# Kernel optimization log

Hardware: AMD Instinct MI355X
Metric: run time of the kernel (lower is better)

The kernel has to match this reference:

```python
import jax, jax.numpy as jnp
import numpy as np

B, NQ, D, NH, L, P = 8, 1000, 256, 8, 4, 4
DFF = 1024
HD = D // NH
SHAPES = np.array([[128, 128], [64, 64], [32, 32], [16, 16]], dtype=np.int64)
S = int((SHAPES[:, 0] * SHAPES[:, 1]).sum())  # 21760
LEVEL_START = np.concatenate([np.zeros(1, np.int64), np.cumsum(SHAPES[:, 0] * SHAPES[:, 1])[:-1]])


def setup_inputs() -> dict:
    key = jax.random.key(0)
    ks = jax.random.split(key, 20)
    w = lambda k, shape, s=0.02: jax.random.normal(k, shape, jnp.float32) * s
    z = lambda n: jnp.zeros((n,), jnp.float32)
    return dict(
        query=w(ks[0], (B, NQ, D), 1.0),
        query_pos=w(ks[1], (B, NQ, D), 1.0),
        reference_points=jax.random.uniform(ks[2], (B, NQ, L, 4), jnp.float32),
        input_flatten=w(ks[3], (B, S, D), 1.0),
        input_spatial_shapes=SHAPES,
        input_level_start_index=LEVEL_START,
        Wq=w(ks[4], (D, D)), bq=z(D), Wk=w(ks[5], (D, D)), bk=z(D),
        Wv=w(ks[6], (D, D)), bv=z(D), Wo=w(ks[7], (D, D)), bo=z(D),
        ln1_g=jnp.ones((D,), jnp.float32), ln1_b=z(D),
        W_off=w(ks[8], (D, NH * L * P * 2)), b_off=z(NH * L * P * 2),
        W_attn=w(ks[9], (D, NH * L * P)), b_attn=z(NH * L * P),
        W_val=w(ks[10], (D, D)), b_val=z(D),
        W_cout=w(ks[11], (D, D)), b_cout=z(D),
        ln2_g=jnp.ones((D,), jnp.float32), ln2_b=z(D),
        W1=w(ks[12], (D, DFF)), b1=z(DFF),
        W2=w(ks[13], (DFF, D)), b2=z(D),
        ln3_g=jnp.ones((D,), jnp.float32), ln3_b=z(D),
    )


def layer_norm(x, g, b, eps=1e-5):
    mu = x.mean(-1, keepdims=True)
    var = ((x - mu) ** 2).mean(-1, keepdims=True)
    return (x - mu) / jnp.sqrt(var + eps) * g + b


def _ms_deform(value, shapes_np, loc, aw):
    # value: (B,S,NH,HD); loc: (B,Nq,NH,L,P,2) in [0,1]; aw: (B,Nq,NH,L,P)
    Bz, _, nh, hd = value.shape
    Nq = loc.shape[1]
    awt = aw.transpose(0, 2, 1, 3, 4)  # (B,NH,Nq,L,P)
    acc = jnp.zeros((Bz, nh, Nq, hd), value.dtype)
    start = 0
    for lvl in range(shapes_np.shape[0]):
        Hl, Wl = int(shapes_np[lvl, 0]), int(shapes_np[lvl, 1])
        vf = value[:, start:start + Hl * Wl].transpose(0, 2, 1, 3)  # (B,NH,Hl*Wl,HD)
        start += Hl * Wl
        # grid_sample align_corners=False: pixel coord = loc * size - 0.5
        lx = loc[:, :, :, lvl, :, 0].transpose(0, 2, 1, 3) * Wl - 0.5  # (B,NH,Nq,P)
        ly = loc[:, :, :, lvl, :, 1].transpose(0, 2, 1, 3) * Hl - 0.5
        x0 = jnp.floor(lx); y0 = jnp.floor(ly)
        tx = lx - x0; ty = ly - y0
        x0i = x0.astype(jnp.int32); y0i = y0.astype(jnp.int32)

        def gather(xi, yi):
            valid = (xi >= 0) & (xi < Wl) & (yi >= 0) & (yi < Hl)
            idx = jnp.clip(yi, 0, Hl - 1) * Wl + jnp.clip(xi, 0, Wl - 1)
            out = jnp.take_along_axis(vf, idx.reshape(Bz, nh, Nq * P)[..., None], axis=2)
            return out.reshape(Bz, nh, Nq, P, hd) * valid[..., None]

        g00 = gather(x0i, y0i)
        g01 = gather(x0i + 1, y0i)
        g10 = gather(x0i, y0i + 1)
        g11 = gather(x0i + 1, y0i + 1)
        samp = (g00 * ((1 - tx) * (1 - ty))[..., None] + g01 * (tx * (1 - ty))[..., None]
                + g10 * ((1 - tx) * ty)[..., None] + g11 * (tx * ty)[..., None])  # (B,NH,Nq,P,HD)
        acc = acc + jnp.einsum('bhqp,bhqpd->bhqd', awt[:, :, :, lvl], samp)
    return acc.transpose(0, 2, 1, 3).reshape(Bz, Nq, nh * hd)


def reference(query, query_pos, reference_points, input_flatten, input_spatial_shapes,
              input_level_start_index, Wq, bq, Wk, bk, Wv, bv, Wo, bo, ln1_g, ln1_b,
              W_off, b_off, W_attn, b_attn, W_val, b_val, W_cout, b_cout, ln2_g, ln2_b,
              W1, b1, W2, b2, ln3_g, ln3_b):
    Bz, Nq, Dm = query.shape
    # --- self-attention (post-norm), pos added to Q/K only ---
    qp = query + query_pos
    q = (qp @ Wq + bq).reshape(Bz, Nq, NH, HD)
    k = (qp @ Wk + bk).reshape(Bz, Nq, NH, HD)
    v = (query @ Wv + bv).reshape(Bz, Nq, NH, HD)
    att = jax.nn.softmax(jnp.einsum('bqhd,bkhd->bhqk', q, k) / jnp.sqrt(jnp.float32(HD)), axis=-1)
    sa = jnp.einsum('bhqk,bkhd->bqhd', att, v).reshape(Bz, Nq, Dm) @ Wo + bo
    x = layer_norm(query + sa, ln1_g, ln1_b)
    # --- deformable cross-attention ---
    q2 = x + query_pos
    value = (input_flatten @ W_val + b_val).reshape(Bz, -1, NH, HD)
    off = (q2 @ W_off + b_off).reshape(Bz, Nq, NH, L, P, 2)
    aw = jax.nn.softmax((q2 @ W_attn + b_attn).reshape(Bz, Nq, NH, L * P), axis=-1)
    aw = aw.reshape(Bz, Nq, NH, L, P)
    rp = reference_points  # (B,Nq,L,4) cxcywh
    loc = rp[:, :, None, :, None, :2] + off / P * rp[:, :, None, :, None, 2:] * 0.5
    shapes_np = np.asarray(input_spatial_shapes)
    ca = _ms_deform(value, shapes_np, loc, aw) @ W_cout + b_cout
    x = layer_norm(x + ca, ln2_g, ln2_b)
    # --- FFN ---
    ffn = jax.nn.relu(x @ W1 + b1) @ W2 + b2
    return layer_norm(x + ffn, ln3_g, ln3_b)
```

## Files before the change

kernel.cpp:

```cpp
#include <hip/hip_runtime.h>
#include <hip/hip_bf16.h>

#define B_   8
#define NQ_  1000
#define D_   256
#define NH_  8
#define L_   4
#define P_   4
#define DFF_ 1024
#define HD_  32
#define S_   21760
#define NTOK (B_*NQ_)

typedef short  bf16x8 __attribute__((ext_vector_type(8)));
typedef float  f32x4  __attribute__((ext_vector_type(4)));

#define WAITBAR(N) asm volatile("s_waitcnt vmcnt(" #N ") lgkmcnt(0)\n\ts_barrier" ::: "memory")
#define ENDBAR()   asm volatile("s_barrier" ::: "memory")

__device__ inline unsigned short f32_to_bf16_bits(float f) {
    unsigned int u = __float_as_uint(f);
    unsigned int rounding = 0x7FFFu + ((u >> 16) & 1u);
    u += rounding;
    return (unsigned short)(u >> 16);
}
__device__ inline float bf16_bits_to_f32(unsigned short b) {
    return __uint_as_float(((unsigned int)b) << 16);
}
__device__ inline unsigned int pack_trunc(float f0, float f1) {
    return __builtin_amdgcn_perm(__float_as_uint(f1), __float_as_uint(f0), 0x07060302u);
}
__device__ inline void async_copy16(const void* g, void* l) {
    __builtin_amdgcn_global_load_lds((const __attribute__((address_space(1))) unsigned int*)g,
                                     (__attribute__((address_space(3))) unsigned int*)l, 16, 0, 0);
}

__global__ __launch_bounds__(256) void vgemm(const float* __restrict__ Af,
                                             const unsigned short* __restrict__ Bt,
                                             const float* __restrict__ bias,
                                             unsigned short* __restrict__ Cb)
{
    constexpr int K = 256;
    constexpr int N = 256;
    __shared__ __align__(16) unsigned short sA[128 * 64];
    __shared__ __align__(16) unsigned short sB[2][128 * 64];
    const int tid = threadIdx.x;
    const int w = tid >> 6, l = tid & 63;
    const int n0 = blockIdx.x * 128, m0 = blockIdx.y * 128;
    const int wr = w >> 1, wc = w & 1;

    f32x4 acc[4][4];
    #pragma unroll
    for (int i = 0; i < 4; i++)
        #pragma unroll
        for (int j = 0; j < 4; j++)
            #pragma unroll
            for (int r = 0; r < 4; r++) acc[i][j][r] = 0.f;

    const int lrow = (tid >> 3);
    const int lko  = (tid & 7) * 8;

    auto issueB = [&](int t, int buf) {
        #pragma unroll
        for (int r = 0; r < 4; r++) {
            int boff = ((r * 4 + w) * 64 + l) * 16;
            int row  = boff >> 7;
            int kb   = (boff & 127) ^ ((row & 7) << 4);
            async_copy16(Bt + (size_t)(n0 + row) * K + t * 64 + (kb >> 1),
                         sB[buf] + (size_t)(r * 4 + w) * 512);
        }
    };
    auto loadA = [&](int t, float4* fr) {
        #pragma unroll
        for (int r = 0; r < 4; r++) {
            int row = r * 32 + lrow;
            const float* ap = Af + (size_t)(m0 + row) * K + t * 64 + lko;
            fr[r * 2]     = *reinterpret_cast<const float4*>(ap);
            fr[r * 2 + 1] = *reinterpret_cast<const float4*>(ap + 4);
        }
    };
    auto writeA = [&](const float4* fr) {
        #pragma unroll
        for (int r = 0; r < 4; r++) {
            int row = r * 32 + lrow;
            float4 a0 = fr[r * 2], a1 = fr[r * 2 + 1];
            uint4 t4;
            t4.x = pack_trunc(a0.x, a0.y);
            t4.y = pack_trunc(a0.z, a0.w);
            t4.z = pack_trunc(a1.x, a1.y);
            t4.w = pack_trunc(a1.z, a1.w);
            int sw = (lko * 2) ^ ((row & 7) << 4);
            *reinterpret_cast<uint4*>(&sA[row * 64 + (sw >> 1)]) = t4;
        }
    };
    auto compute = [&](int buf) {
        const unsigned short* sBc = sB[buf];
        #pragma unroll
        for (int kk = 0; kk < 2; kk++) {
            bf16x8 afr[4], bfr[4];
            const int kbyte = kk * 64 + ((l >> 4) << 4);
            #pragma unroll
            for (int mi = 0; mi < 4; mi++) {
                int row = wr * 64 + mi * 16 + (l & 15);
                int sw = kbyte ^ ((row & 7) << 4);
                afr[mi] = *reinterpret_cast<const bf16x8*>(&sA[row * 64 + (sw >> 1)]);
            }
            #pragma unroll
            for (int ni = 0; ni < 4; ni++) {
                int row = wc * 64 + ni * 16 + (l & 15);
                int sw = kbyte ^ ((row & 7) << 4);
                bfr[ni] = *reinterpret_cast<const bf16x8*>(&sBc[row * 64 + (sw >> 1)]);
            }
            #pragma unroll
            for (int mi = 0; mi < 4; mi++)
                #pragma unroll
                for (int ni = 0; ni < 4; ni++)
                    acc[mi][ni] = __builtin_amdgcn_mfma_f32_16x16x32_bf16(
                        afr[mi], bfr[ni], acc[mi][ni], 0, 0, 0);
        }
    };

    float4 frA[8], frB[8];

    loadA(0, frA);
    issueB(0, 0);
    loadA(1, frB);

    writeA(frA);
    issueB(1, 1);
    loadA(2, frA);
    WAITBAR(20);
    compute(0);
    ENDBAR();
    writeA(frB);
    issueB(2, 0);
    loadA(3, frB);
    WAITBAR(20);
    compute(1);
    ENDBAR();
    writeA(frA);
    issueB(3, 1);
    WAITBAR(12);
    compute(0);
    ENDBAR();
    writeA(frB);
    WAITBAR(0);
    compute(1);
    ENDBAR();

    #pragma unroll
    for (int mi = 0; mi < 4; mi++) {
        #pragma unroll
        for (int ni = 0; ni < 4; ni++) {
            int col = n0 + wc * 64 + ni * 16 + (l & 15);
            float bz = bias[col];
            #pragma unroll
            for (int rg = 0; rg < 4; rg++) {
                int row = m0 + wr * 64 + mi * 16 + ((l >> 4) << 2) + rg;
                Cb[(size_t)row * N + col] = f32_to_bf16_bits(acc[mi][ni][rg] + bz);
            }
        }
    }
}

template<int AMODE, bool RELU, int CMODE, int BN, int K, int NSTRIP>
__global__ __launch_bounds__(256) void bgemm(const void* __restrict__ Av,
                                             const float* __restrict__ A2,
                                             const unsigned short* __restrict__ Bt,
                                             const float* __restrict__ bias,
                                             float* __restrict__ Cf,
                                             unsigned short* __restrict__ Cb,
                                             int N)
{
    constexpr int NF   = BN / 16;
    constexpr int KF   = K / 32;
    constexpr int ROWB = K * 2;
    constexpr int FILL = BN * ROWB / 4096;

    __shared__ __align__(16) unsigned short sB[BN * K];

    const int tid = threadIdx.x;
    const int w = tid >> 6, l = tid & 63;
    const int g = l >> 4, lr = l & 15;
    const int n0 = blockIdx.x * BN;

    const unsigned short* Ab = (const unsigned short*)Av;
    const float* Af = (const float*)Av;

    #pragma unroll
    for (int r = 0; r < FILL; r++) {
        int lin = (r * 256 + tid) * 16;
        int row = lin / ROWB;
        int kb  = (lin & (ROWB - 1)) ^ ((row & 7) << 4);
        async_copy16(Bt + (size_t)(n0 + row) * K + (kb >> 1), (char*)sB + lin);
    }
    asm volatile("s_waitcnt vmcnt(0)\n\ts_barrier" ::: "memory");

    float bz[NF];
    #pragma unroll
    for (int nf = 0; nf < NF; nf++) bz[nf] = bias[n0 + nf * 16 + lr];

    for (int s = 0; s < NSTRIP; s++) {
        const int m0w = (blockIdx.y * NSTRIP + s) * 64 + w * 16;
        const int arow = m0w + lr;

        f32x4 acc[NF];
        #pragma unroll
        for (int nf = 0; nf < NF; nf++)
            #pragma unroll
            for (int r = 0; r < 4; r++) acc[nf][r] = 0.f;

        #pragma unroll
        for (int kf = 0; kf < KF; kf++) {
            bf16x8 af;
            if constexpr (AMODE == 0) {
                af = *reinterpret_cast<const bf16x8*>(Ab + (size_t)arow * K + kf * 32 + g * 8);
            } else {
                const float* ap = Af + (size_t)arow * K + kf * 32 + g * 8;
                float4 a0 = *reinterpret_cast<const float4*>(ap);
                float4 a1 = *reinterpret_cast<const float4*>(ap + 4);
                if constexpr (AMODE == 2) {
                    const float* a2 = A2 + (size_t)arow * K + kf * 32 + g * 8;
                    float4 b0 = *reinterpret_cast<const float4*>(a2);
                    float4 b1 = *reinterpret_cast<const float4*>(a2 + 4);
                    a0.x += b0.x; a0.y += b0.y; a0.z += b0.z; a0.w += b0.w;
                    a1.x += b1.x; a1.y += b1.y; a1.z += b1.z; a1.w += b1.w;
                }
                uint4 t;
                t.x = pack_trunc(a0.x, a0.y);
                t.y = pack_trunc(a0.z, a0.w);
                t.z = pack_trunc(a1.x, a1.y);
                t.w = pack_trunc(a1.z, a1.w);
                af = *reinterpret_cast<bf16x8*>(&t);
            }
            #pragma unroll
            for (int nf = 0; nf < NF; nf++) {
                int brow = nf * 16 + lr;
                bf16x8 bf = *reinterpret_cast<const bf16x8*>(
                    (const char*)sB + brow * ROWB + ((kf * 64 + g * 16) ^ ((brow & 7) << 4)));
                acc[nf] = __builtin_amdgcn_mfma_f32_16x16x32_bf16(af, bf, acc[nf], 0, 0, 0);
            }
        }

        #pragma unroll
        for (int nf = 0; nf < NF; nf++) {
            int col = n0 + nf * 16 + lr;
            if constexpr (CMODE == 2) {
                int row0 = m0w + g * 4;
                int bb = row0 / 1000;
                int key = row0 - bb * 1000;
                ushort4 q4;
                q4.x = f32_to_bf16_bits(acc[nf][0] + bz[nf]);
                q4.y = f32_to_bf16_bits(acc[nf][1] + bz[nf]);
                q4.z = f32_to_bf16_bits(acc[nf][2] + bz[nf]);
                q4.w = f32_to_bf16_bits(acc[nf][3] + bz[nf]);
                *reinterpret_cast<ushort4*>(Cb + (size_t)bb * 262144 + (size_t)col * 1024 + key) = q4;
            } else {
                #pragma unroll
                for (int rg = 0; rg < 4; rg++) {
                    int row = m0w + g * 4 + rg;
                    float v = acc[nf][rg] + bz[nf];
                    if (RELU) v = fmaxf(v, 0.f);
                    if constexpr (CMODE == 1)
                        Cb[(size_t)row * N + col] = f32_to_bf16_bits(v);
                    else
                        Cf[(size_t)row * N + col] = v;
                }
            }
        }
    }
}

struct WJobs {
    const float* src[10];
    unsigned short* dst[10];
    int K[10], N[10];
};
__global__ __launch_bounds__(256) void wconv_k(WJobs j)
{
    const int job = blockIdx.y;
    const int K = j.K[job], N = j.N[job];
    const int tilesN = N >> 6;
    const int ntiles = (K >> 6) * tilesN;
    const int tile = blockIdx.x;
    if (tile >= ntiles) return;
    const int kt = tile / tilesN, nt = tile - kt * tilesN;
    const int k0 = kt * 64, n0 = nt * 64;
    __shared__ unsigned short t_[64][65];
    const float* src = j.src[job];
    unsigned short* dst = j.dst[job];
    const int cc = threadIdx.x & 63, rr = threadIdx.x >> 6;
    #pragma unroll
    for (int i = 0; i < 16; i++) {
        int k = i * 4 + rr;
        t_[k][cc] = f32_to_bf16_bits(src[(size_t)(k0 + k) * N + n0 + cc]);
    }
    __syncthreads();
    #pragma unroll
    for (int i = 0; i < 16; i++) {
        int n = i * 4 + rr;
        dst[(size_t)(n0 + n) * K + k0 + cc] = t_[cc][n];
    }
}

__global__ __launch_bounds__(1024) void biaspack_k(const float* bq, const float* bk,
                                                   const float* boff, const float* battn,
                                                   float* qkb, float* oab)
{
    int t = threadIdx.x;
    if (t < 256)      qkb[t] = bq[t];
    else if (t < 512) qkb[t] = bk[t - 256];
    else if (t < 768) oab[t - 512] = boff[t - 512];
    else if (t < 896) oab[t - 512] = battn[t - 768];
}

__global__ __launch_bounds__(256) void fattn_k(const unsigned short* __restrict__ qk,
                                               const unsigned short* __restrict__ vt,
                                               unsigned short* __restrict__ sa)
{
    const int b = blockIdx.z, h = blockIdx.y;
    const int tid = threadIdx.x;
    const int w = tid >> 6, l = tid & 63;
    const int lq = l & 15, g = l >> 4;
    const int q0 = blockIdx.x * 64 + w * 16;

    __shared__ __align__(16) unsigned short Ks[2][128 * 32];
    __shared__ __align__(16) unsigned short Vs[2][32 * 128];
    __shared__ __align__(16) unsigned short Ps[4][16 * 128];

    int qrow = q0 + lq; if (qrow > NQ_ - 1) qrow = NQ_ - 1;
    const bf16x8 qfrag = *reinterpret_cast<const bf16x8*>(
        qk + ((size_t)(b * NQ_ + qrow)) * 512 + h * 32 + g * 8);

    f32x4 O0 = {0.f, 0.f, 0.f, 0.f}, O1 = {0.f, 0.f, 0.f, 0.f};
    float m = -1e30f, lsum = 0.f;
    const float scale = 0.17677669529663687f;

    const size_t kbase = (size_t)b * (NQ_ * 512) + 256 + h * 32;
    const size_t vbase = (size_t)b * 262144 + (size_t)(h * 32) * 1024;
    const int swz = (lq & 7) << 4;

    auto issueKV = [&](int kt, int buf) {
        #pragma unroll
        for (int r = 0; r < 2; r++) {
            int lin = (r * 256 + tid) * 16;
            int krow = lin >> 6;
            int kb = (lin & 63) ^ ((krow & 7) << 4);
            async_copy16(qk + kbase + (size_t)(kt * 128 + krow) * 512 + (kb >> 1),
                         (char*)Ks[buf] + lin);
            int d = lin >> 8;
            int vb = (lin & 255) ^ ((d & 7) << 4);
            async_copy16(vt + vbase + (size_t)d * 1024 + kt * 128 + (vb >> 1),
                         (char*)Vs[buf] + lin);
        }
    };

    issueKV(0, 0);

    for (int kt = 0; kt < 8; kt++) {
        const int k0 = kt * 128;
        const int cur = kt & 1;
        asm volatile("s_waitcnt vmcnt(0) lgkmcnt(0)\n\ts_barrier" ::: "memory");
        if (kt < 7) issueKV(kt + 1, cur ^ 1);

        const unsigned short* Kc = Ks[cur];
        const unsigned short* Vc = Vs[cur];

        float t[8][4];
        float tmax = -1e30f;
        const bool tail = (k0 + 128 > NQ_);
        #pragma unroll
        for (int ni = 0; ni < 8; ni++) {
            int row = ni * 16 + lq;
            bf16x8 kf = *reinterpret_cast<const bf16x8*>(
                (const char*)Kc + row * 64 + ((g * 16) ^ swz));
            f32x4 st = __builtin_amdgcn_mfma_f32_16x16x32_bf16(
                kf, qfrag, (f32x4){0.f, 0.f, 0.f, 0.f}, 0, 0, 0);
            #pragma unroll
            for (int rg = 0; rg < 4; rg++) {
                float tv = st[rg] * scale;
                if (tail) {
                    int key = k0 + ni * 16 + g * 4 + rg;
                    tv = (key < NQ_) ? tv : -1e30f;
                }
                t[ni][rg] = tv;
                tmax = fmaxf(tmax, tv);
            }
        }
        tmax = fmaxf(tmax, __shfl_xor(tmax, 16));
        tmax = fmaxf(tmax, __shfl_xor(tmax, 32));
        float mnew = fmaxf(m, tmax);
        float corr = __expf(m - mnew);
        m = mnew;

        float rs = 0.f;
        unsigned int pk[8][2];
        #pragma unroll
        for (int ni = 0; ni < 8; ni++) {
            float p0 = __expf(t[ni][0] - mnew);
            float p1 = __expf(t[ni][1] - mnew);
            float p2 = __expf(t[ni][2] - mnew);
            float p3 = __expf(t[ni][3] - mnew);
            rs += (p0 + p1) + (p2 + p3);
            pk[ni][0] = ((unsigned)f32_to_bf16_bits(p0)) | (((unsigned)f32_to_bf16_bits(p1)) << 16);
            pk[ni][1] = ((unsigned)f32_to_bf16_bits(p2)) | (((unsigned)f32_to_bf16_bits(p3)) << 16);
        }
        rs += __shfl_xor(rs, 16);
        rs += __shfl_xor(rs, 32);
        lsum = lsum * corr + rs;

        float c0 = __shfl(corr, g * 4 + 0);
        float c1 = __shfl(corr, g * 4 + 1);
        float c2 = __shfl(corr, g * 4 + 2);
        float c3 = __shfl(corr, g * 4 + 3);
        O0[0] *= c0; O0[1] *= c1; O0[2] *= c2; O0[3] *= c3;
        O1[0] *= c0; O1[1] *= c1; O1[2] *= c2; O1[3] *= c3;

        unsigned short* Pw = Ps[w];
        #pragma unroll
        for (int ni = 0; ni < 8; ni++) {
            int byteoff = lq * 256 + ((ni * 32 + g * 8) ^ swz);
            *reinterpret_cast<uint2*>((char*)Pw + byteoff) = make_uint2(pk[ni][0], pk[ni][1]);
        }

        #pragma unroll
        for (int c = 0; c < 4; c++) {
            int rb = (c * 64 + g * 16) ^ swz;
            bf16x8 pa = *reinterpret_cast<const bf16x8*>((const char*)Pw + lq * 256 + rb);
            bf16x8 v0 = *reinterpret_cast<const bf16x8*>((const char*)Vc + lq * 256 + rb);
            bf16x8 v1 = *reinterpret_cast<const bf16x8*>((const char*)Vc + (16 + lq) * 256 + rb);
            O0 = __builtin_amdgcn_mfma_f32_16x16x32_bf16(pa, v0, O0, 0, 0, 0);
            O1 = __builtin_amdgcn_mfma_f32_16x16x32_bf16(pa, v1, O1, 0, 0, 0);
        }
    }

    float linv = 1.f / lsum;
    float i0 = __shfl(linv, g * 4 + 0);
    float i1 = __shfl(linv, g * 4 + 1);
    float i2 = __shfl(linv, g * 4 + 2);
    float i3 = __shfl(linv, g * 4 + 3);
    float iv[4] = {i0, i1, i2, i3};
    #pragma unroll
    for (int rg = 0; rg < 4; rg++) {
        int qg = q0 + g * 4 + rg;
        if (qg < NQ_) {
            size_t obase = ((size_t)(b * NQ_ + qg)) * 256 + h * 32;
            sa[obase + lq]      = f32_to_bf16_bits(O0[rg] * iv[rg]);
            sa[obase + 16 + lq] = f32_to_bf16_bits(O1[rg] * iv[rg]);
        }
    }
}

__global__ __launch_bounds__(256) void ln_k(const float* __restrict__ a,
                                            const float* __restrict__ bsum,
                                            const float* __restrict__ g,
                                            const float* __restrict__ be,
                                            float* __restrict__ out)
{
    const int wave = threadIdx.x >> 6, lane = threadIdx.x & 63;
    const int row = blockIdx.x * 4 + wave;
    float4 xa = reinterpret_cast<const float4*>(a + (size_t)row * 256)[lane];
    float4 xb = reinterpret_cast<const float4*>(bsum + (size_t)row * 256)[lane];
    float4 x = {xa.x + xb.x, xa.y + xb.y, xa.z + xb.z, xa.w + xb.w};
    float s  = x.x + x.y + x.z + x.w;
    float ss = x.x * x.x + x.y * x.y + x.z * x.z + x.w * x.w;
    #pragma unroll
    for (int off = 32; off > 0; off >>= 1) {
        s  += __shfl_xor(s, off);
        ss += __shfl_xor(ss, off);
    }
    float mu  = s * (1.f / 256.f);
    float var = ss * (1.f / 256.f) - mu * mu;
    float rstd = rsqrtf(var + 1e-5f);
    float4 gv = reinterpret_cast<const float4*>(g)[lane];
    float4 bv = reinterpret_cast<const float4*>(be)[lane];
    float4 o = {(x.x - mu) * rstd * gv.x + bv.x,
                (x.y - mu) * rstd * gv.y + bv.y,
                (x.z - mu) * rstd * gv.z + bv.z,
                (x.w - mu) * rstd * gv.w + bv.w};
    reinterpret_cast<float4*>(out + (size_t)row * 256)[lane] = o;
}

__device__ inline unsigned int samp2(const unsigned short* __restrict__ v,
                                     int b, int st, int Wl, int Hl,
                                     int x, int y, int hc)
{
    bool valid = (x >= 0) & (x < Wl) & (y >= 0) & (y < Hl);
    int xc = min(max(x, 0), Wl - 1);
    int yc = min(max(y, 0), Hl - 1);
    size_t idx = ((size_t)(b * S_ + st + yc * Wl + xc)) * 256 + hc;
    unsigned int val = *reinterpret_cast<const unsigned int*>(v + idx);
    return valid ? val : 0u;
}

__global__ __launch_bounds__(256) void deform_k(const float* __restrict__ rp,
                                                const float* __restrict__ oa,
                                                const unsigned short* __restrict__ value,
                                                unsigned short* __restrict__ ca)
{
    const int tk = threadIdx.x >> 7;
    const int tok = blockIdx.x * 2 + tk;
    const int b = tok / NQ_;
    const int h = (threadIdx.x >> 4) & 7;
    const int cp = threadIdx.x & 15;
    const int hc = h * 32 + cp * 2;

    const float* awp = oa + (size_t)tok * 384 + 256 + h * 16;
    float w[16];
    float mx = -1e30f;
    #pragma unroll
    for (int i = 0; i < 16; i++) { w[i] = awp[i]; mx = fmaxf(mx, w[i]); }
    float sum = 0.f;
    #pragma unroll
    for (int i = 0; i < 16; i++) { w[i] = __expf(w[i] - mx); sum += w[i]; }
    const float inv = 1.f / sum;

    const float* rpp  = rp + (size_t)tok * (L_ * 4);
    const float* offp = oa + (size_t)tok * 384 + h * 32;

    const int lvlW[4] = {128, 64, 32, 16};
    const int lvlS[4] = {0, 16384, 20480, 21504};

    float acc0 = 0.f, acc1 = 0.f;
    #pragma unroll
    for (int l = 0; l < 4; l++) {
        const int Wl = lvlW[l], Hl = lvlW[l], st = lvlS[l];
        const float cx = rpp[l * 4 + 0], cy = rpp[l * 4 + 1];
        const float cw = rpp[l * 4 + 2], chh = rpp[l * 4 + 3];
        #pragma unroll
        for (int p = 0; p < 4; p++) {
            float ox = offp[l * 8 + p * 2 + 0];
            float oy = offp[l * 8 + p * 2 + 1];
            float lx = (cx + ox * 0.25f * cw * 0.5f) * Wl - 0.5f;
            float ly = (cy + oy * 0.25f * chh * 0.5f) * Hl - 0.5f;
            float x0f = floorf(lx), y0f = floorf(ly);
            float tx = lx - x0f, ty = ly - y0f;
            int x0 = (int)x0f, y0 = (int)y0f;
            unsigned int u00 = samp2(value, b, st, Wl, Hl, x0,     y0,     hc);
            unsigned int u01 = samp2(value, b, st, Wl, Hl, x0 + 1, y0,     hc);
            unsigned int u10 = samp2(value, b, st, Wl, Hl, x0,     y0 + 1, hc);
            unsigned int u11 = samp2(value, b, st, Wl, Hl, x0 + 1, y0 + 1, hc);
            float w00 = (1.f - tx) * (1.f - ty), w01 = tx * (1.f - ty);
            float w10 = (1.f - tx) * ty,         w11 = tx * ty;
            float g0 = bf16_bits_to_f32((unsigned short)u00) * w00
                     + bf16_bits_to_f32((unsigned short)u01) * w01
                     + bf16_bits_to_f32((unsigned short)u10) * w10
                     + bf16_bits_to_f32((unsigned short)u11) * w11;
            float g1 = bf16_bits_to_f32((unsigned short)(u00 >> 16)) * w00
                     + bf16_bits_to_f32((unsigned short)(u01 >> 16)) * w01
                     + bf16_bits_to_f32((unsigned short)(u10 >> 16)) * w10
                     + bf16_bits_to_f32((unsigned short)(u11 >> 16)) * w11;
            float wa = w[l * 4 + p] * inv;
            acc0 += wa * g0;
            acc1 += wa * g1;
        }
    }
    unsigned int packed = ((unsigned)f32_to_bf16_bits(acc0)) | (((unsigned)f32_to_bf16_bits(acc1)) << 16);
    *reinterpret_cast<unsigned int*>(ca + (size_t)tok * 256 + hc) = packed;
}

extern "C" void kernel_launch(void* const* d_in, const int* in_sizes, int n_in,
                              void* d_out, int out_size, void* d_ws, size_t ws_size,
                              hipStream_t stream)
{
    const float* query      = (const float*)d_in[0];
    const float* query_pos  = (const float*)d_in[1];
    const float* ref_pts    = (const float*)d_in[2];
    const float* input_flat = (const float*)d_in[3];
    const float* Wq = (const float*)d_in[6];  const float* bq = (const float*)d_in[7];
    const float* Wk = (const float*)d_in[8];  const float* bk = (const float*)d_in[9];
    const float* Wv = (const float*)d_in[10]; const float* bv = (const float*)d_in[11];
    const float* Wo = (const float*)d_in[12]; const float* bo = (const float*)d_in[13];
    const float* ln1g = (const float*)d_in[14]; const float* ln1b = (const float*)d_in[15];
    const float* W_off = (const float*)d_in[16]; const float* b_off = (const float*)d_in[17];
    const float* W_attn = (const float*)d_in[18]; const float* b_attn = (const float*)d_in[19];
    const float* W_val = (const float*)d_in[20]; const float* b_val = (const float*)d_in[21];
    const float* W_cout = (const float*)d_in[22]; const float* b_cout = (const float*)d_in[23];
    const float* ln2g = (const float*)d_in[24]; const float* ln2b = (const float*)d_in[25];
    const float* W1 = (const float*)d_in[26]; const float* b1 = (const float*)d_in[27];
    const float* W2 = (const float*)d_in[28]; const float* b2 = (const float*)d_in[29];
    const float* ln3g = (const float*)d_in[30]; const float* ln3b = (const float*)d_in[31];
    float* out = (float*)d_out;

    char* base = (char*)d_ws;
    size_t off = 0;
    auto alloc = [&](size_t bytes) { void* p = base + off; off += (bytes + 255) & ~(size_t)255; return p; };
    unsigned short* value_bf = (unsigned short*)alloc((size_t)B_ * S_ * 256 * 2);
    unsigned short* qk_bf = (unsigned short*)alloc((size_t)NTOK * 1024 * 2);
    unsigned short* h_bf = qk_bf;
    unsigned short* vt = (unsigned short*)alloc((size_t)B_ * 256 * 1024 * 2);
    float* oa_buf = (float*)alloc((size_t)NTOK * 384 * 4);
    float* tmp0   = (float*)alloc((size_t)NTOK * 256 * 4);
    float* x1     = (float*)alloc((size_t)NTOK * 256 * 4);
    float* x2     = (float*)alloc((size_t)NTOK * 256 * 4);
    unsigned short* sc_bf = (unsigned short*)alloc((size_t)NTOK * 256 * 2);
    unsigned short* wqk   = (unsigned short*)alloc(512 * 256 * 2);
    unsigned short* wv    = (unsigned short*)alloc(256 * 256 * 2);
    unsigned short* wo    = (unsigned short*)alloc(256 * 256 * 2);
    unsigned short* woa   = (unsigned short*)alloc(384 * 256 * 2);
    unsigned short* wval  = (unsigned short*)alloc(256 * 256 * 2);
    unsigned short* wcout = (unsigned short*)alloc(256 * 256 * 2);
    unsigned short* w1t   = (unsigned short*)alloc(1024 * 256 * 2);
    unsigned short* w2t   = (unsigned short*)alloc(256 * 1024 * 2);
    float* qkbias = (float*)alloc(512 * 4);
    float* oabias = (float*)alloc(384 * 4);

    dim3 blk(256);

    WJobs wj;
    wj.src[0] = Wq;    wj.dst[0] = wqk;               wj.K[0] = 256;  wj.N[0] = 256;
    wj.src[1] = Wk;    wj.dst[1] = wqk + 256 * 256;   wj.K[1] = 256;  wj.N[1] = 256;
    wj.src[2] = Wv;    wj.dst[2] = wv;                wj.K[2] = 256;  wj.N[2] = 256;
    wj.src[3] = Wo;    wj.dst[3] = wo;                wj.K[3] = 256;  wj.N[3] = 256;
    wj.src[4] = W_off; wj.dst[4] = woa;               wj.K[4] = 256;  wj.N[4] = 256;
    wj.src[5] = W_attn;wj.dst[5] = woa + 256 * 256;   wj.K[5] = 256;  wj.N[5] = 128;
    wj.src[6] = W_val; wj.dst[6] = wval;              wj.K[6] = 256;  wj.N[6] = 256;
    wj.src[7] = W_cout;wj.dst[7] = wcout;             wj.K[7] = 256;  wj.N[7] = 256;
    wj.src[8] = W1;    wj.dst[8] = w1t;               wj.K[8] = 256;  wj.N[8] = 1024;
    wj.src[9] = W2;    wj.dst[9] = w2t;               wj.K[9] = 1024; wj.N[9] = 256;
    wconv_k<<<dim3(64, 10), blk, 0, stream>>>(wj);
    biaspack_k<<<1, 1024, 0, stream>>>(bq, bk, b_off, b_attn, qkbias, oabias);

    bgemm<2, false, 1,  64, 256, 1><<<dim3(8, 125), blk, 0, stream>>>(query, query_pos, wqk, qkbias, nullptr, qk_bf, 512);
    bgemm<1, false, 2,  64, 256, 1><<<dim3(4, 125), blk, 0, stream>>>(query, nullptr,   wv,  bv,     nullptr, vt,    256);
    fattn_k<<<dim3(16, NH_, B_), blk, 0, stream>>>(qk_bf, vt, sc_bf);
    bgemm<0, false, 0,  64, 256, 1><<<dim3(4, 125), blk, 0, stream>>>(sc_bf, nullptr, wo, bo, tmp0, nullptr, 256);
    ln_k<<<NTOK / 4, blk, 0, stream>>>(query, tmp0, ln1g, ln1b, x1);

    vgemm<<<dim3(2, 1360), blk, 0, stream>>>(input_flat, wval, b_val, value_bf);
    bgemm<2, false, 0,  64, 256, 1><<<dim3(6, 125), blk, 0, stream>>>(x1, query_pos, woa, oabias, oa_buf, nullptr, 384);
    deform_k<<<NTOK / 2, blk, 0, stream>>>(ref_pts, oa_buf, value_bf, sc_bf);
    bgemm<0, false, 0,  64, 256, 1><<<dim3(4, 125), blk, 0, stream>>>(sc_bf, nullptr, wcout, b_cout, tmp0, nullptr, 256);
    ln_k<<<NTOK / 4, blk, 0, stream>>>(x1, tmp0, ln2g, ln2b, x2);

    bgemm<1, true,  1,  64, 256, 1><<<dim3(16, 125), blk, 0, stream>>>(x2, nullptr, w1t, b1, nullptr, h_bf, 1024);
    bgemm<0, false, 0,  32, 1024, 1><<<dim3(8, 125), blk, 0, stream>>>(h_bf, nullptr, w2t, b2, tmp0, nullptr, 256);
    ln_k<<<NTOK / 4, blk, 0, stream>>>(x2, tmp0, ln3g, ln3b, out);
}
```

Baseline: 278.5 us.

## Pre-convert GEMM activations to bf16 in a merged prep kernel and layernorm epilogues

Adds a single prep kernel that merges weight transposition, bias packing, conversion of input_flatten to bf16, and bf16 conversion of query and query+pos. Layernorm kernels now also emit bf16 copies (x1+pos, x2) for the next GEMM. This lets every GEMM read bf16 A operands directly, and vgemm loads A asynchronously into LDS with a simple double-buffered loop. The aim is to cut fp32 A traffic and in-kernel conversion, at the cost of an extra full pass that writes and rereads a bf16 copy of input_flatten (~89MB).

```diff
diff --git a/kernel.cpp b/kernel.cpp
--- a/kernel.cpp
+++ b/kernel.cpp
@@ -35,14 +35,89 @@
                                      (__attribute__((address_space(3))) unsigned int*)l, 16, 0, 0);
 }
 
-__global__ __launch_bounds__(256) void vgemm(const float* __restrict__ Af,
-                                             const unsigned short* __restrict__ Bt,
-                                             const float* __restrict__ bias,
-                                             unsigned short* __restrict__ Cb)
+struct PrepArgs {
+    const float* wsrc[10];
+    unsigned short* wdst[10];
+    int wK[10], wN[10];
+    const float* bq; const float* bk; const float* boff; const float* battn;
+    float* qkb; float* oab;
+    const float* input_flat; unsigned short* if_bf;
+    const float* query; const float* qpos;
+    unsigned short* q_bf; unsigned short* qp_bf;
+};
+__global__ __launch_bounds__(256) void prep_k(PrepArgs P)
+{
+    const int bid = blockIdx.x, tid = threadIdx.x;
+    if (bid < 640) {
+        const int job = bid >> 6, tile = bid & 63;
+        const int K = P.wK[job], N = P.wN[job];
+        const int tilesN = N >> 6;
+        if (tile >= (K >> 6) * tilesN) return;
+        const int kt = tile / tilesN, nt = tile - kt * tilesN;
+        const int k0 = kt * 64, n0 = nt * 64;
+        __shared__ unsigned short t_[64][65];
+        const float* src = P.wsrc[job];
+        unsigned short* dst = P.wdst[job];
+        const int cc = tid & 63, rr = tid >> 6;
+        #pragma unroll
+        for (int i = 0; i < 16; i++) {
+            int k = i * 4 + rr;
+            t_[k][cc] = f32_to_bf16_bits(src[(size_t)(k0 + k) * N + n0 + cc]);
+        }
+        __syncthreads();
+        #pragma unroll
+        for (int i = 0; i < 16; i++) {
+            int n = i * 4 + rr;
+            dst[(size_t)(n0 + n) * K + k0 + cc] = t_[cc][n];
+        }
+    } else if (bid < 2816) {
+        int idx = (bid - 640) * 256 + tid;
+        for (int i = idx; i < 5570560; i += 2176 * 256) {
+            const float* p = P.input_flat + (size_t)i * 8;
+            float4 a0 = *reinterpret_cast<const float4*>(p);
+            float4 a1 = *reinterpret_cast<const float4*>(p + 4);
+            uint4 t;
+            t.x = pack_trunc(a0.x, a0.y);
+            t.y = pack_trunc(a0.z, a0.w);
+            t.z = pack_trunc(a1.x, a1.y);
+            t.w = pack_trunc(a1.z, a1.w);
+            *reinterpret_cast<uint4*>(P.if_bf + (size_t)i * 8) = t;
+        }
+    } else if (bid == 2816) {
+        P.qkb[tid]       = P.bq[tid];
+        P.qkb[256 + tid] = P.bk[tid];
+        P.oab[tid]       = P.boff[tid];
+        if (tid < 128) P.oab[256 + tid] = P.battn[tid];
+    } else {
+        int idx = (bid - 2817) * 256 + tid;
+        for (int i = idx; i < 256000; i += 64 * 256) {
+            const float* q = P.query + (size_t)i * 8;
+            const float* p = P.qpos  + (size_t)i * 8;
+            float4 q0 = *reinterpret_cast<const float4*>(q);
+            float4 q1 = *reinterpret_cast<const float4*>(q + 4);
+            float4 p0 = *reinterpret_cast<const float4*>(p);
+            float4 p1 = *reinterpret_cast<const float4*>(p + 4);
+            uint4 tq, tp;
+            tq.x = pack_trunc(q0.x, q0.y);       tq.y = pack_trunc(q0.z, q0.w);
+            tq.z = pack_trunc(q1.x, q1.y);       tq.w = pack_trunc(q1.z, q1.w);
+            tp.x = pack_trunc(q0.x + p0.x, q0.y + p0.y);
+            tp.y = pack_trunc(q0.z + p0.z, q0.w + p0.w);
+            tp.z = pack_trunc(q1.x + p1.x, q1.y + p1.y);
+            tp.w = pack_trunc(q1.z + p1.z, q1.w + p1.w);
+            *reinterpret_cast<uint4*>(P.q_bf  + (size_t)i * 8) = tq;
+            *reinterpret_cast<uint4*>(P.qp_bf + (size_t)i * 8) = tp;
+        }
+    }
+}
+
+__global__ __launch_bounds__(256) void vgemm0(const unsigned short* __restrict__ Ab,
+                                              const unsigned short* __restrict__ Bt,
+                                              const float* __restrict__ bias,
+                                              unsigned short* __restrict__ Cb)
 {
     constexpr int K = 256;
     constexpr int N = 256;
-    __shared__ __align__(16) unsigned short sA[128 * 64];
+    __shared__ __align__(16) unsigned short sA[2][128 * 64];
     __shared__ __align__(16) unsigned short sB[2][128 * 64];
     const int tid = threadIdx.x;
     const int w = tid >> 6, l = tid & 63;
@@ -57,9 +132,16 @@
             #pragma unroll
             for (int r = 0; r < 4; r++) acc[i][j][r] = 0.f;
 
-    const int lrow = (tid >> 3);
-    const int lko  = (tid & 7) * 8;
-
+    auto issueA = [&](int t, int buf) {
+        #pragma unroll
+        for (int r = 0; r < 4; r++) {
+            int boff = ((r * 4 + w) * 64 + l) * 16;
+            int row  = boff >> 7;
+            int kb   = (boff & 127) ^ ((row & 7) << 4);
+            async_copy16(Ab + (size_t)(m0 + row) * K + t * 64 + (kb >> 1),
+                         sA[buf] + (size_t)(r * 4 + w) * 512);
+        }
+    };
     auto issueB = [&](int t, int buf) {
         #pragma unroll
         for (int r = 0; r < 4; r++) {
@@ -70,31 +152,19 @@
                          sB[buf] + (size_t)(r * 4 + w) * 512);
         }
     };
-    auto loadA = [&](int t, float4* fr) {
-        #pragma unroll
-        for (int r = 0; r < 4; r++) {
-            int row = r * 32 + lrow;
-            const float* ap = Af + (size_t)(m0 + row) * K + t * 64 + lko;
-            fr[r * 2]     = *reinterpret_cast<const float4*>(ap);
-            fr[r * 2 + 1] = *reinterpret_cast<const float4*>(ap + 4);
-        }
-    };
-    auto writeA = [&](const float4* fr) {
-        #pragma unroll
-        for (int r = 0; r < 4; r++) {
-            int row = r * 32 + lrow;
-            float4 a0 = fr[r * 2], a1 = fr[r * 2 + 1];
-            uint4 t4;
-            t4.x = pack_trunc(a0.x, a0.y);
-            t4.y = pack_trunc(a0.z, a0.w);
-            t4.z = pack_trunc(a1.x, a1.y);
-            t4.w = pack_trunc(a1.z, a1.w);
-            int sw = (lko * 2) ^ ((row & 7) << 4);
-            *reinterpret_cast<uint4*>(&sA[row * 64 + (sw >> 1)]) = t4;
-        }
-    };
-    auto compute = [&](int buf) {
-        const unsigned short* sBc = sB[buf];
+
+    issueA(0, 0);
+    issueB(0, 0);
+
+    for (int t = 0; t < 4; t++) {
+        const int cur = t & 1;
+        if (t + 1 < 4) {
+            issueA(t + 1, cur ^ 1);
+            issueB(t + 1, cur ^ 1);
+            WAITBAR(8);
+        } else {
+            WAITBAR(0);
+        }
         #pragma unroll
         for (int kk = 0; kk < 2; kk++) {
             bf16x8 afr[4], bfr[4];
@@ -103,13 +173,13 @@
             for (int mi = 0; mi < 4; mi++) {
                 int row = wr * 64 + mi * 16 + (l & 15);
                 int sw = kbyte ^ ((row & 7) << 4);
-                afr[mi] = *reinterpret_cast<const bf16x8*>(&sA[row * 64 + (sw >> 1)]);
+                afr[mi] = *reinterpret_cast<const bf16x8*>(&sA[cur][row * 64 + (sw >> 1)]);
             }
             #pragma unroll
             for (int ni = 0; ni < 4; ni++) {
                 int row = wc * 64 + ni * 16 + (l & 15);
                 int sw = kbyte ^ ((row & 7) << 4);
-                bfr[ni] = *reinterpret_cast<const bf16x8*>(&sBc[row * 64 + (sw >> 1)]);
+                bfr[ni] = *reinterpret_cast<const bf16x8*>(&sB[cur][row * 64 + (sw >> 1)]);
             }
             #pragma unroll
             for (int mi = 0; mi < 4; mi++)
@@ -118,35 +188,8 @@
                     acc[mi][ni] = __builtin_amdgcn_mfma_f32_16x16x32_bf16(
                         afr[mi], bfr[ni], acc[mi][ni], 0, 0, 0);
         }
-    };
-
-    float4 frA[8], frB[8];
-
-    loadA(0, frA);
-    issueB(0, 0);
-    loadA(1, frB);
-
-    writeA(frA);
-    issueB(1, 1);
-    loadA(2, frA);
-    WAITBAR(20);
-    compute(0);
-    ENDBAR();
-    writeA(frB);
-    issueB(2, 0);
-    loadA(3, frB);
-    WAITBAR(20);
-    compute(1);
-    ENDBAR();
-    writeA(frA);
-    issueB(3, 1);
-    WAITBAR(12);
-    compute(0);
-    ENDBAR();
-    writeA(frB);
-    WAITBAR(0);
-    compute(1);
-    ENDBAR();
+        ENDBAR();
+    }
 
     #pragma unroll
     for (int mi = 0; mi < 4; mi++) {
@@ -163,9 +206,8 @@
     }
 }
 
-template<int AMODE, bool RELU, int CMODE, int BN, int K, int NSTRIP>
-__global__ __launch_bounds__(256) void bgemm(const void* __restrict__ Av,
-                                             const float* __restrict__ A2,
+template<bool RELU, int CMODE, int BN, int K>
+__global__ __launch_bounds__(256) void bgemm(const unsigned short* __restrict__ Ab,
                                              const unsigned short* __restrict__ Bt,
                                              const float* __restrict__ bias,
                                              float* __restrict__ Cf,
@@ -184,9 +226,6 @@
     const int g = l >> 4, lr = l & 15;
     const int n0 = blockIdx.x * BN;
 
-    const unsigned short* Ab = (const unsigned short*)Av;
-    const float* Af = (const float*)Av;
-
     #pragma unroll
     for (int r = 0; r < FILL; r++) {
         int lin = (r * 256 + tid) * 16;
@@ -200,118 +239,53 @@
     #pragma unroll
     for (int nf = 0; nf < NF; nf++) bz[nf] = bias[n0 + nf * 16 + lr];
 
-    for (int s = 0; s < NSTRIP; s++) {
-        const int m0w = (blockIdx.y * NSTRIP + s) * 64 + w * 16;
-        const int arow = m0w + lr;
-
-        f32x4 acc[NF];
-        #pragma unroll
-        for (int nf = 0; nf < NF; nf++)
+    const int m0w = blockIdx.y * 64 + w * 16;
+    const int arow = m0w + lr;
+
+    f32x4 acc[NF];
+    #pragma unroll
+    for (int nf = 0; nf < NF; nf++)
+        #pragma unroll
+        for (int r = 0; r < 4; r++) acc[nf][r] = 0.f;
+
+    #pragma unroll
+    for (int kf = 0; kf < KF; kf++) {
+        bf16x8 af = *reinterpret_cast<const bf16x8*>(Ab + (size_t)arow * K + kf * 32 + g * 8);
+        #pragma unroll
+        for (int nf = 0; nf < NF; nf++) {
+            int brow = nf * 16 + lr;
+            bf16x8 bf = *reinterpret_cast<const bf16x8*>(
+                (const char*)sB + brow * ROWB + ((kf * 64 + g * 16) ^ ((brow & 7) << 4)));
+            acc[nf] = __builtin_amdgcn_mfma_f32_16x16x32_bf16(af, bf, acc[nf], 0, 0, 0);
+        }
+    }
+
+    #pragma unroll
+    for (int nf = 0; nf < NF; nf++) {
+        int col = n0 + nf * 16 + lr;
+        if constexpr (CMODE == 2) {
+            int row0 = m0w + g * 4;
+            int bb = row0 / 1000;
+            int key = row0 - bb * 1000;
+            ushort4 q4;
+            q4.x = f32_to_bf16_bits(acc[nf][0] + bz[nf]);
+            q4.y = f32_to_bf16_bits(acc[nf][1] + bz[nf]);
+            q4.z = f32_to_bf16_bits(acc[nf][2] + bz[nf]);
+            q4.w = f32_to_bf16_bits(acc[nf][3] + bz[nf]);
+            *reinterpret_cast<ushort4*>(Cb + (size_t)bb * 262144 + (size_t)col * 1024 + key) = q4;
+        } else {
             #pragma unroll
-            for (int r = 0; r < 4; r++) acc[nf][r] = 0.f;
-
-        #pragma unroll
-        for (int kf = 0; kf < KF; kf++) {
-            bf16x8 af;
-            if constexpr (AMODE == 0) {
-                af = *reinterpret_cast<const bf16x8*>(Ab + (size_t)arow * K + kf * 32 + g * 8);
-            } else {
-                const float* ap = Af + (size_t)arow * K + kf * 32 + g * 8;
-                float4 a0 = *reinterpret_cast<const float4*>(ap);
-                float4 a1 = *reinterpret_cast<const float4*>(ap + 4);
-                if constexpr (AMODE == 2) {
-                    const float* a2 = A2 + (size_t)arow * K + kf * 32 + g * 8;
-                    float4 b0 = *reinterpret_cast<const float4*>(a2);
-                    float4 b1 = *reinterpret_cast<const float4*>(a2 + 4);
-                    a0.x += b0.x; a0.y += b0.y; a0.z += b0.z; a0.w += b0.w;
-                    a1.x += b1.x; a1.y += b1.y; a1.z += b1.z; a1.w += b1.w;
-                }
-                uint4 t;
-                t.x = pack_trunc(a0.x, a0.y);
-                t.y = pack_trunc(a0.z, a0.w);
-                t.z = pack_trunc(a1.x, a1.y);
-                t.w = pack_trunc(a1.z, a1.w);
-                af = *reinterpret_cast<bf16x8*>(&t);
+            for (int rg = 0; rg < 4; rg++) {
+                int row = m0w + g * 4 + rg;
+                float v = acc[nf][rg] + bz[nf];
+                if (RELU) v = fmaxf(v, 0.f);
+                if constexpr (CMODE == 1)
+                    Cb[(size_t)row * N + col] = f32_to_bf16_bits(v);
+                else
+                    Cf[(size_t)row * N + col] = v;
             }
-            #pragma unroll
-            for (int nf = 0; nf < NF; nf++) {
-                int brow = nf * 16 + lr;
-                bf16x8 bf = *reinterpret_cast<const bf16x8*>(
-                    (const char*)sB + brow * ROWB + ((kf * 64 + g * 16) ^ ((brow & 7) << 4)));
-                acc[nf] = __builtin_amdgcn_mfma_f32_16x16x32_bf16(af, bf, acc[nf], 0, 0, 0);
-            }
-        }
-
-        #pragma unroll
-        for (int nf = 0; nf < NF; nf++) {
-            int col = n0 + nf * 16 + lr;
-            if constexpr (CMODE == 2) {
-                int row0 = m0w + g * 4;
-                int bb = row0 / 1000;
-                int key = row0 - bb * 1000;
-                ushort4 q4;
-                q4.x = f32_to_bf16_bits(acc[nf][0] + bz[nf]);
-                q4.y = f32_to_bf16_bits(acc[nf][1] + bz[nf]);
-                q4.z = f32_to_bf16_bits(acc[nf][2] + bz[nf]);
-                q4.w = f32_to_bf16_bits(acc[nf][3] + bz[nf]);
-                *reinterpret_cast<ushort4*>(Cb + (size_t)bb * 262144 + (size_t)col * 1024 + key) = q4;
-            } else {
-                #pragma unroll
-                for (int rg = 0; rg < 4; rg++) {
-                    int row = m0w + g * 4 + rg;
-                    float v = acc[nf][rg] + bz[nf];
-                    if (RELU) v = fmaxf(v, 0.f);
-                    if constexpr (CMODE == 1)
-                        Cb[(size_t)row * N + col] = f32_to_bf16_bits(v);
-                    else
-                        Cf[(size_t)row * N + col] = v;
-                }
-            }
-        }
-    }
-}
-
-struct WJobs {
-    const float* src[10];
-    unsigned short* dst[10];
-    int K[10], N[10];
-};
-__global__ __launch_bounds__(256) void wconv_k(WJobs j)
-{
-    const int job = blockIdx.y;
-    const int K = j.K[job], N = j.N[job];
-    const int tilesN = N >> 6;
-    const int ntiles = (K >> 6) * tilesN;
-    const int tile = blockIdx.x;
-    if (tile >= ntiles) return;
-    const int kt = tile / tilesN, nt = tile - kt * tilesN;
-    const int k0 = kt * 64, n0 = nt * 64;
-    __shared__ unsigned short t_[64][65];
-    const float* src = j.src[job];
-    unsigned short* dst = j.dst[job];
-    const int cc = threadIdx.x & 63, rr = threadIdx.x >> 6;
-    #pragma unroll
-    for (int i = 0; i < 16; i++) {
-        int k = i * 4 + rr;
-        t_[k][cc] = f32_to_bf16_bits(src[(size_t)(k0 + k) * N + n0 + cc]);
-    }
-    __syncthreads();
-    #pragma unroll
-    for (int i = 0; i < 16; i++) {
-        int n = i * 4 + rr;
-        dst[(size_t)(n0 + n) * K + k0 + cc] = t_[cc][n];
-    }
-}
-
-__global__ __launch_bounds__(1024) void biaspack_k(const float* bq, const float* bk,
-                                                   const float* boff, const float* battn,
-                                                   float* qkb, float* oab)
-{
-    int t = threadIdx.x;
-    if (t < 256)      qkb[t] = bq[t];
-    else if (t < 512) qkb[t] = bk[t - 256];
-    else if (t < 768) oab[t - 512] = boff[t - 512];
-    else if (t < 896) oab[t - 512] = battn[t - 768];
+        }
+    }
 }
 
 __global__ __launch_bounds__(256) void fattn_k(const unsigned short* __restrict__ qk,
@@ -451,11 +425,14 @@
     }
 }
 
+template<int OM>
 __global__ __launch_bounds__(256) void ln_k(const float* __restrict__ a,
                                             const float* __restrict__ bsum,
+                                            const float* __restrict__ pos,
                                             const float* __restrict__ g,
                                             const float* __restrict__ be,
-                                            float* __restrict__ out)
+                                            float* __restrict__ out,
+                                            unsigned short* __restrict__ outb)
 {
     const int wave = threadIdx.x >> 6, lane = threadIdx.x & 63;
     const int row = blockIdx.x * 4 + wave;
@@ -479,6 +456,18 @@
                 (x.z - mu) * rstd * gv.z + bv.z,
                 (x.w - mu) * rstd * gv.w + bv.w};
     reinterpret_cast<float4*>(out + (size_t)row * 256)[lane] = o;
+    if constexpr (OM == 1) {
+        ushort4 q4;
+        q4.x = f32_to_bf16_bits(o.x); q4.y = f32_to_bf16_bits(o.y);
+        q4.z = f32_to_bf16_bits(o.z); q4.w = f32_to_bf16_bits(o.w);
+        *reinterpret_cast<ushort4*>(outb + (size_t)row * 256 + lane * 4) = q4;
+    } else if constexpr (OM == 2) {
+        float4 pv = reinterpret_cast<const float4*>(pos + (size_t)row * 256)[lane];
+        ushort4 q4;
+        q4.x = f32_to_bf16_bits(o.x + pv.x); q4.y = f32_to_bf16_bits(o.y + pv.y);
+        q4.z = f32_to_bf16_bits(o.z + pv.z); q4.w = f32_to_bf16_bits(o.w + pv.w);
+        *reinterpret_cast<ushort4*>(outb + (size_t)row * 256 + lane * 4) = q4;
+    }
 }
 
 __device__ inline unsigned int samp2(const unsigned short* __restrict__ v,
@@ -586,6 +575,7 @@
     size_t off = 0;
     auto alloc = [&](size_t bytes) { void* p = base + off; off += (bytes + 255) & ~(size_t)255; return p; };
     unsigned short* value_bf = (unsigned short*)alloc((size_t)B_ * S_ * 256 * 2);
+    unsigned short* if_bf = (unsigned short*)alloc((size_t)B_ * S_ * 256 * 2);
     unsigned short* qk_bf = (unsigned short*)alloc((size_t)NTOK * 1024 * 2);
     unsigned short* h_bf = qk_bf;
     unsigned short* vt = (unsigned short*)alloc((size_t)B_ * 256 * 1024 * 2);
@@ -593,7 +583,11 @@
     float* tmp0   = (float*)alloc((size_t)NTOK * 256 * 4);
     float* x1     = (float*)alloc((size_t)NTOK * 256 * 4);
     float* x2     = (float*)alloc((size_t)NTOK * 256 * 4);
-    unsigned short* sc_bf = (unsigned short*)alloc((size_t)NTOK * 256 * 2);
+    unsigned short* sc_bf  = (unsigned short*)alloc((size_t)NTOK * 256 * 2);
+    unsigned short* q_bf   = (unsigned short*)alloc((size_t)NTOK * 256 * 2);
+    unsigned short* qp_bf  = (unsigned short*)alloc((size_t)NTOK * 256 * 2);
+    unsigned short* x1p_bf = (unsigned short*)alloc((size_t)NTOK * 256 * 2);
+    unsigned short* x2_bf  = (unsigned short*)alloc((size_t)NTOK * 256 * 2);
     unsigned short* wqk   = (unsigned short*)alloc(512 * 256 * 2);
     unsigned short* wv    = (unsigned short*)alloc(256 * 256 * 2);
     unsigned short* wo    = (unsigned short*)alloc(256 * 256 * 2);
@@ -607,33 +601,36 @@
 
     dim3 blk(256);
 
-    WJobs wj;
-    wj.src[0] = Wq;    wj.dst[0] = wqk;               wj.K[0] = 256;  wj.N[0] = 256;
-    wj.src[1] = Wk;    wj.dst[1] = wqk + 256 * 256;   wj.K[1] = 256;  wj.N[1] = 256;
-    wj.src[2] = Wv;    wj.dst[2] = wv;                wj.K[2] = 256;  wj.N[2] = 256;
-    wj.src[3] = Wo;    wj.dst[3] = wo;                wj.K[3] = 256;  wj.N[3] = 256;
-    wj.src[4] = W_off; wj.dst[4] = woa;               wj.K[4] = 256;  wj.N[4] = 256;
-    wj.src[5] = W_attn;wj.dst[5] = woa + 256 * 256;   wj.K[5] = 256;  wj.N[5] = 128;
-    wj.src[6] = W_val; wj.dst[6] = wval;              wj.K[6] = 256;  wj.N[6] = 256;
-    wj.src[7] = W_cout;wj.dst[7] = wcout;             wj.K[7] = 256;  wj.N[7] = 256;
-    wj.src[8] = W1;    wj.dst[8] = w1t;               wj.K[8] = 256;  wj.N[8] = 1024;
-    wj.src[9] = W2;    wj.dst[9] = w2t;               wj.K[9] = 1024; wj.N[9] = 256;
-    wconv_k<<<dim3(64, 10), blk, 0, stream>>>(wj);
-    biaspack_k<<<1, 1024, 0, stream>>>(bq, bk, b_off, b_attn, qkbias, oabias);
-
-    bgemm<2, false, 1,  64, 256, 1><<<dim3(8, 125), blk, 0, stream>>>(query, query_pos, wqk, qkbias, nullptr, qk_bf, 512);
-    bgemm<1, false, 2,  64, 256, 1><<<dim3(4, 125), blk, 0, stream>>>(query, nullptr,   wv,  bv,     nullptr, vt,    256);
+    PrepArgs P;
+    P.wsrc[0] = Wq;    P.wdst[0] = wqk;               P.wK[0] = 256;  P.wN[0] = 256;
+    P.wsrc[1] = Wk;    P.wdst[1] = wqk + 256 * 256;   P.wK[1] = 256;  P.wN[1] = 256;
+    P.wsrc[2] = Wv;    P.wdst[2] = wv;                P.wK[2] = 256;  P.wN[2] = 256;
+    P.wsrc[3] = Wo;    P.wdst[3] = wo;                P.wK[3] = 256;  P.wN[3] = 256;
+    P.wsrc[4] = W_off; P.wdst[4] = woa;               P.wK[4] = 256;  P.wN[4] = 256;
+    P.wsrc[5] = W_attn;P.wdst[5] = woa + 256 * 256;   P.wK[5] = 256;  P.wN[5] = 128;
+    P.wsrc[6] = W_val; P.wdst[6] = wval;              P.wK[6] = 256;  P.wN[6] = 256;
+    P.wsrc[7] = W_cout;P.wdst[7] = wcout;             P.wK[7] = 256;  P.wN[7] = 256;
+    P.wsrc[8] = W1;    P.wdst[8] = w1t;               P.wK[8] = 256;  P.wN[8] = 1024;
+    P.wsrc[9] = W2;    P.wdst[9] = w2t;               P.wK[9] = 1024; P.wN[9] = 256;
+    P.bq = bq; P.bk = bk; P.boff = b_off; P.battn = b_attn;
+    P.qkb = qkbias; P.oab = oabias;
+    P.input_flat = input_flat; P.if_bf = if_bf;
+    P.query = query; P.qpos = query_pos; P.q_bf = q_bf; P.qp_bf = qp_bf;
+    prep_k<<<2881, blk, 0, stream>>>(P);
+
+    bgemm<false, 1,  64, 256><<<dim3(8, 125), blk, 0, stream>>>(qp_bf, wqk, qkbias, nullptr, qk_bf, 512);
+    bgemm<false, 2,  64, 256><<<dim3(4, 125), blk, 0, stream>>>(q_bf,  wv,  bv,     nullptr, vt,    256);
     fattn_k<<<dim3(16, NH_, B_), blk, 0, stream>>>(qk_bf, vt, sc_bf);
-    bgemm<0, false, 0,  64, 256, 1><<<dim3(4, 125), blk, 0, stream>>>(sc_bf, nullptr, wo, bo, tmp0, nullptr, 256);
-    ln_k<<<NTOK / 4, blk, 0, stream>>>(query, tmp0, ln1g, ln1b, x1);
-
-    vgemm<<<dim3(2, 1360), blk, 0, stream>>>(input_flat, wval, b_val, value_bf);
-    bgemm<2, false, 0,  64, 256, 1><<<dim3(6, 125), blk, 0, stream>>>(x1, query_pos, woa, oabias, oa_buf, nullptr, 384);
+    bgemm<false, 0,  64, 256><<<dim3(4, 125), blk, 0, stream>>>(sc_bf, wo, bo, tmp0, nullptr, 256);
+    ln_k<2><<<NTOK / 4, blk, 0, stream>>>(query, tmp0, query_pos, ln1g, ln1b, x1, x1p_bf);
+
+    vgemm0<<<dim3(2, 1360), blk, 0, stream>>>(if_bf, wval, b_val, value_bf);
+    bgemm<false, 0,  64, 256><<<dim3(6, 125), blk, 0, stream>>>(x1p_bf, woa, oabias, oa_buf, nullptr, 384);
     deform_k<<<NTOK / 2, blk, 0, stream>>>(ref_pts, oa_buf, value_bf, sc_bf);
-    bgemm<0, false, 0,  64, 256, 1><<<dim3(4, 125), blk, 0, stream>>>(sc_bf, nullptr, wcout, b_cout, tmp0, nullptr, 256);
-    ln_k<<<NTOK / 4, blk, 0, stream>>>(x1, tmp0, ln2g, ln2b, x2);
-
-    bgemm<1, true,  1,  64, 256, 1><<<dim3(16, 125), blk, 0, stream>>>(x2, nullptr, w1t, b1, nullptr, h_bf, 1024);
-    bgemm<0, false, 0,  32, 1024, 1><<<dim3(8, 125), blk, 0, stream>>>(h_bf, nullptr, w2t, b2, tmp0, nullptr, 256);
-    ln_k<<<NTOK / 4, blk, 0, stream>>>(x2, tmp0, ln3g, ln3b, out);
-}
+    bgemm<false, 0,  64, 256><<<dim3(4, 125), blk, 0, stream>>>(sc_bf, wcout, b_cout, tmp0, nullptr, 256);
+    ln_k<1><<<NTOK / 4, blk, 0, stream>>>(x1, tmp0, nullptr, ln2g, ln2b, x2, x2_bf);
+
+    bgemm<true,  1,  64, 256><<<dim3(16, 125), blk, 0, stream>>>(x2_bf, w1t, b1, nullptr, h_bf, 1024);
+    bgemm<false, 0,  32, 1024><<<dim3(8, 125), blk, 0, stream>>>(h_bf, w2t, b2, tmp0, nullptr, 256);
+    ln_k<0><<<NTOK / 4, blk, 0, stream>>>(x2, tmp0, nullptr, ln3g, ln3b, out, nullptr);
+}
```

After: 286.0 us. +2.7%, slower.
